# Kernel tuning notes

Hardware: AMD Instinct MI355X
Metric: run time of the kernel (lower is better)

Reference implementation:

```python
import jax, jax.numpy as jnp
import numpy as np

Y_SCALE = 1.0   # from init_kwargs
EPS = 1e-12     # matches torch F.normalize eps


def _l2_normalize(x):
    n = jnp.linalg.norm(x, axis=-1, keepdims=True)
    return x / jnp.maximum(n, EPS)


def _sequence_similarity(a, b):
    # a: [B, N, D], b: [B, M, D]
    a = _l2_normalize(a)
    b = _l2_normalize(b)
    cos_sims = jnp.einsum('bnd,bmd->bnm', a, b)  # [B, N, M]
    if cos_sims.shape[-1] > cos_sims.shape[-2]:
        max_sims = cos_sims.max(axis=-1)  # [B, N]
    else:
        max_sims = cos_sims.max(axis=-2)  # [B, M]
    return max_sims.mean(axis=-1)  # [B]


def setup_inputs() -> dict:
    key = jax.random.key(0)
    k1, k2, k3 = jax.random.split(key, 3)
    B, N, M, D = 16, 4096, 2048, 256
    x1 = jax.random.normal(k1, (B, N, D), dtype=jnp.float32)
    x2 = jax.random.normal(k2, (B, M, D), dtype=jnp.float32)
    y = jax.random.uniform(k3, (B,), dtype=jnp.float32)
    return {"x1": x1, "x2": x2, "y": y}


def reference(x1, x2, y):
    raw_sim_scores = _sequence_similarity(x1, x2)  # [B]
    losses = (raw_sim_scores - y) ** 2
    scales = jnp.where(y != 0.0, jnp.float32(Y_SCALE), jnp.float32(1.0))
    return (losses * scales).sum()
```

## Files before the change

### kernel.cpp

```cpp
#include <hip/hip_runtime.h>
#include <hip/hip_bf16.h>
#include <cstdint>
#include <cstddef>

#define BATCH 16
#define NROWS 4096
#define MROWS 2048
#define DDIM  256
#define NSPLIT 2
#define NCHUNKS 8

typedef __attribute__((ext_vector_type(8)))  int   i32x8;
typedef __attribute__((ext_vector_type(16))) float f32x16;

__global__ void __launch_bounds__(256) norm_cast(
    const float* __restrict__ x1, const float* __restrict__ x2,
    unsigned char* __restrict__ aout, unsigned char* __restrict__ bout) {
  const int wid  = threadIdx.x >> 6;
  const int lane = threadIdx.x & 63;
  const long long row = (long long)blockIdx.x * 4 + wid;
  const long long R1 = (long long)BATCH * NROWS;
  const long long R2 = (long long)BATCH * MROWS;
  if (row >= R1 + R2) return;
  const float* src; unsigned char* dst;
  if (row < R1) { src = x1 + row * DDIM; dst = aout + row * DDIM; }
  else { long long r2 = row - R1; src = x2 + r2 * DDIM; dst = bout + r2 * DDIM; }
  float4 v = ((const float4*)src)[lane];
  float ss = v.x*v.x + v.y*v.y + v.z*v.z + v.w*v.w;
  #pragma unroll
  for (int o = 32; o >= 1; o >>= 1) ss += __shfl_xor(ss, o, 64);
  float sc = 1.0f / fmaxf(sqrtf(ss), 1e-12f);
  int r = __builtin_amdgcn_cvt_pk_fp8_f32(v.x * sc, v.y * sc, 0, false);
  r = __builtin_amdgcn_cvt_pk_fp8_f32(v.z * sc, v.w * sc, r, true);
  ((unsigned int*)dst)[lane] = (unsigned int)r;
}

typedef __attribute__((address_space(1))) const void gas_t;
typedef __attribute__((address_space(3))) void las_t;
#define GLL16(g, l) __builtin_amdgcn_global_lds((gas_t*)(g), (las_t*)(l), 16, 0, 0)
#undef GLL16
#define GLL16(g, l) __builtin_amdgcn_global_load_lds((gas_t*)(g), (las_t*)(l), 16, 0, 0)

#define LDSA(S) (lds + ((S) << 14))
#define LDSB(S) (lds + 65536 + ((S) << 14))

static __device__ __forceinline__ i32x8 frag8(const char* slot, int row, int lane) {
  const int rb = (lane >> 1) & 3;
  const int ks = lane >> 5;
  const char* base = slot + row * 64;
  uint4 u0 = *(const uint4*)(base + ((((ks << 1) | 0) ^ rb) << 4));
  uint4 u1 = *(const uint4*)(base + ((((ks << 1) | 1) ^ rb) << 4));
  i32x8 r;
  r[0] = u0.x; r[1] = u0.y; r[2] = u0.z; r[3] = u0.w;
  r[4] = u1.x; r[5] = u1.y; r[6] = u1.z; r[7] = u1.w;
  return r;
}

__global__ void __launch_bounds__(512, 1) maxsim_fp8(
    const unsigned char* __restrict__ A,
    const unsigned char* __restrict__ Bm,
    float* __restrict__ partials)
{
  __shared__ __align__(16) char lds[131072];

  const int t = threadIdx.x;
  const int lane = t & 63;
  const int w = t >> 6;
  const int wr = w >> 2;
  const int wc = w & 3;
  const int l31 = lane & 31;

  const int hw = blockIdx.x;
  const int logical = (hw & 7) * 32 + (hw >> 3);
  const int mt = logical & 7;
  const int grp = logical >> 3;
  const int sp = grp & 1;
  const int bb = grp >> 1;

  const int m0 = mt * 256;
  const int nbase = sp * (NROWS / NSPLIT);

  const unsigned char* Aba = A  + (size_t)bb * NROWS * DDIM;
  const unsigned char* Bba = Bm + ((size_t)bb * MROWS + m0) * DDIM;

  const int r0 = (w * 2 + 0) * 16 + (lane >> 2);
  const int r1 = (w * 2 + 1) * 16 + (lane >> 2);
  const int sph = (((lane & 3) ^ ((lane >> 3) & 3)) << 4);
  const unsigned char* sA0 = Aba + (size_t)r0 * DDIM + sph;
  const unsigned char* sA1 = Aba + (size_t)r1 * DDIM + sph;
  const unsigned char* sB0 = Bba + (size_t)r0 * DDIM + sph;
  const unsigned char* sB1 = Bba + (size_t)r1 * DDIM + sph;
  const int l0 = (w * 2 + 0) * 1024 + lane * 16;
  const int l1 = (w * 2 + 1) * 1024 + lane * 16;

  #define STAGE_A(SLOT, OFF) do { \
    GLL16(sA0 + (OFF), (SLOT) + l0); GLL16(sA1 + (OFF), (SLOT) + l1); } while (0)
  #define STAGE_B(SLOT, OFF) do { \
    GLL16(sB0 + (OFF), (SLOT) + l0); GLL16(sB1 + (OFF), (SLOT) + l1); } while (0)

  f32x16 acc[4][2] = {};
  const f32x16 z16 = {};
  i32x8 af[4], bf[2];
  float cm[2] = {-INFINITY, -INFINITY};

  STAGE_A(LDSA(0), (size_t)nbase * DDIM + 0);
  STAGE_B(LDSB(0), 0);
  STAGE_B(LDSB(1), 64);
  STAGE_B(LDSB(2), 128);
  STAGE_B(LDSB(3), 192);
  STAGE_A(LDSA(1), (size_t)nbase * DDIM + 64);
  asm volatile("s_waitcnt vmcnt(8)" ::: "memory");
  asm volatile("s_barrier" ::: "memory");

  for (int nc = 0; nc < NCHUNKS; ++nc) {
    #pragma unroll
    for (int kt = 0; kt < 4; ++kt) {
      const char* sa = LDSA(kt);
      const char* sb = LDSB(kt);
      const int s2 = (kt + 2) & 3;
      const int nc2 = (kt < 2) ? nc : ((nc + 1) & (NCHUNKS - 1));
      const size_t offA2 = ((size_t)nbase + nc2 * 256) * DDIM + s2 * 64;

      #pragma unroll
      for (int nj = 0; nj < 2; ++nj)
        bf[nj] = frag8(sb, wc * 64 + nj * 32 + l31, lane);
      #pragma unroll
      for (int mi = 0; mi < 4; ++mi)
        af[mi] = frag8(sa, wr * 128 + mi * 32 + l31, lane);
      STAGE_A(LDSA(s2), offA2);
      #pragma unroll
      for (int mi = 0; mi < 4; ++mi)
        #pragma unroll
        for (int nj = 0; nj < 2; ++nj)
          acc[mi][nj] = __builtin_amdgcn_mfma_scale_f32_32x32x64_f8f6f4(
              af[mi], bf[nj], acc[mi][nj], 0, 0,
              0, 0x7F7F7F7F, 0, 0x7F7F7F7F);
      asm volatile("s_waitcnt vmcnt(2)" ::: "memory");
      asm volatile("s_barrier" ::: "memory");
    }
    #pragma unroll
    for (int nj = 0; nj < 2; ++nj) {
      float v = cm[nj];
      #pragma unroll
      for (int mi = 0; mi < 4; ++mi) {
        #pragma unroll
        for (int r = 0; r < 16; ++r) v = fmaxf(v, acc[mi][nj][r]);
        acc[mi][nj] = z16;
      }
      cm[nj] = v;
    }
  }

  asm volatile("s_waitcnt vmcnt(0)" ::: "memory");
  asm volatile("s_barrier" ::: "memory");
  #pragma unroll
  for (int nj = 0; nj < 2; ++nj)
    cm[nj] = fmaxf(cm[nj], __shfl_xor(cm[nj], 32, 64));
  float* cmax = (float*)lds;
  if (lane < 32) {
    cmax[wr * 256 + wc * 64 + l31]      = cm[0];
    cmax[wr * 256 + wc * 64 + 32 + l31] = cm[1];
  }
  __syncthreads();
  if (t < 256) {
    float v = fmaxf(cmax[t], cmax[256 + t]);
    partials[((size_t)sp * BATCH + bb) * MROWS + m0 + t] = v;
  }
}

__global__ void __launch_bounds__(256) batch_loss(
    const float* __restrict__ partials, const float* __restrict__ y,
    float* __restrict__ bloss) {
  __shared__ float red[4];
  const int b = blockIdx.x;
  const int t = threadIdx.x;
  const int lane = t & 63;
  const int w = t >> 6;
  float s = 0.0f;
  for (int m = t; m < MROWS; m += 256) {
    float v = partials[(size_t)b * MROWS + m];
    #pragma unroll
    for (int sp = 1; sp < NSPLIT; ++sp)
      v = fmaxf(v, partials[((size_t)sp * BATCH + b) * MROWS + m]);
    s += v;
  }
  #pragma unroll
  for (int o = 32; o >= 1; o >>= 1) s += __shfl_xor(s, o, 64);
  if (lane == 0) red[w] = s;
  __syncthreads();
  if (t == 0) {
    float sum = red[0] + red[1] + red[2] + red[3];
    float mean = sum / (float)MROWS;
    float yb = y[b];
    float d = mean - yb;
    bloss[b] = d * d;
  }
}

__global__ void __launch_bounds__(64) final_sum(
    const float* __restrict__ bloss, float* __restrict__ out) {
  const int t = threadIdx.x;
  float v = (t < BATCH) ? bloss[t] : 0.0f;
  #pragma unroll
  for (int o = 32; o >= 1; o >>= 1) v += __shfl_xor(v, o, 64);
  if (t == 0) out[0] = v;
}

extern "C" void kernel_launch(void* const* d_in, const int* in_sizes, int n_in,
                              void* d_out, int out_size, void* d_ws, size_t ws_size,
                              hipStream_t stream) {
  const float* x1 = (const float*)d_in[0];
  const float* x2 = (const float*)d_in[1];
  const float* y  = (const float*)d_in[2];
  float* out = (float*)d_out;

  unsigned char* aF8 = (unsigned char*)d_ws;
  unsigned char* bF8 = aF8 + (size_t)BATCH * NROWS * DDIM;
  float* partials = (float*)(bF8 + (size_t)BATCH * MROWS * DDIM);
  float* bloss = partials + (size_t)NSPLIT * BATCH * MROWS;

  const int totRows = BATCH * (NROWS + MROWS);
  norm_cast<<<(totRows + 3) / 4, 256, 0, stream>>>(x1, x2, aF8, bF8);
  maxsim_fp8<<<BATCH * 8 * NSPLIT, 512, 0, stream>>>(aF8, bF8, partials);
  batch_loss<<<BATCH, 256, 0, stream>>>(partials, y, bloss);
  final_sum<<<1, 64, 0, stream>>>(bloss, out);
}
```

Baseline: 54.16 us.

## Double-buffer LDS fragments in registers and deepen A prefetch to three stages

Deepens the global-to-LDS prefetch of A from two to three k-slices ahead. Adds ping-pong register fragment buffers so the LDS reads for the next k-tile are issued before the MFMAs of the current one, hiding LDS read latency behind matrix math. This costs more VGPRs and tightens the slot-reuse timing. A slot being overwritten while still being read would be a correctness hazard, since only one barrier per k-tile protects it.

```diff
diff --git a/kernel.cpp b/kernel.cpp
--- a/kernel.cpp
+++ b/kernel.cpp
@@ -37,8 +37,6 @@
 
 typedef __attribute__((address_space(1))) const void gas_t;
 typedef __attribute__((address_space(3))) void las_t;
-#define GLL16(g, l) __builtin_amdgcn_global_lds((gas_t*)(g), (las_t*)(l), 16, 0, 0)
-#undef GLL16
 #define GLL16(g, l) __builtin_amdgcn_global_load_lds((gas_t*)(g), (las_t*)(l), 16, 0, 0)
 
 #define LDSA(S) (lds + ((S) << 14))
@@ -100,7 +98,7 @@
 
   f32x16 acc[4][2] = {};
   const f32x16 z16 = {};
-  i32x8 af[4], bf[2];
+  i32x8 afP[4], bfP[2], afQ[4], bfQ[2];
   float cm[2] = {-INFINITY, -INFINITY};
 
   STAGE_A(LDSA(0), (size_t)nbase * DDIM + 0);
@@ -109,35 +107,45 @@
   STAGE_B(LDSB(2), 128);
   STAGE_B(LDSB(3), 192);
   STAGE_A(LDSA(1), (size_t)nbase * DDIM + 64);
-  asm volatile("s_waitcnt vmcnt(8)" ::: "memory");
+  STAGE_A(LDSA(2), (size_t)nbase * DDIM + 128);
+  asm volatile("s_waitcnt vmcnt(2)" ::: "memory");
   asm volatile("s_barrier" ::: "memory");
 
+  #pragma unroll
+  for (int nj = 0; nj < 2; ++nj)
+    bfP[nj] = frag8(LDSB(0), wc * 64 + nj * 32 + l31, lane);
+  #pragma unroll
+  for (int mi = 0; mi < 4; ++mi)
+    afP[mi] = frag8(LDSA(0), wr * 128 + mi * 32 + l31, lane);
+
+  #define KTILE(KT, CAF, CBF, NAF, NBF) do {                                       \
+    const int s3 = ((KT) + 3) & 3;                                                 \
+    const int nc3 = ((KT) == 0) ? nc : ((nc + 1) & (NCHUNKS - 1));                 \
+    const size_t offA3 = ((size_t)nbase + nc3 * 256) * DDIM + s3 * 64;             \
+    STAGE_A(LDSA(s3), offA3);                                                      \
+    const int s1 = ((KT) + 1) & 3;                                                 \
+    _Pragma("unroll")                                                              \
+    for (int nj = 0; nj < 2; ++nj)                                                 \
+      NBF[nj] = frag8(LDSB(s1), wc * 64 + nj * 32 + l31, lane);                    \
+    _Pragma("unroll")                                                              \
+    for (int mi = 0; mi < 4; ++mi)                                                 \
+      NAF[mi] = frag8(LDSA(s1), wr * 128 + mi * 32 + l31, lane);                   \
+    _Pragma("unroll")                                                              \
+    for (int mi = 0; mi < 4; ++mi)                                                 \
+      _Pragma("unroll")                                                            \
+      for (int nj = 0; nj < 2; ++nj)                                               \
+        acc[mi][nj] = __builtin_amdgcn_mfma_scale_f32_32x32x64_f8f6f4(             \
+            CAF[mi], CBF[nj], acc[mi][nj], 0, 0,                                   \
+            0, 0x7F7F7F7F, 0, 0x7F7F7F7F);              \
+    asm volatile("s_waitcnt vmcnt(2)" ::: "memory");                               \
+    asm volatile("s_barrier" ::: "memory");                                        \
+  } while (0)
+
   for (int nc = 0; nc < NCHUNKS; ++nc) {
-    #pragma unroll
-    for (int kt = 0; kt < 4; ++kt) {
-      const char* sa = LDSA(kt);
-      const char* sb = LDSB(kt);
-      const int s2 = (kt + 2) & 3;
-      const int nc2 = (kt < 2) ? nc : ((nc + 1) & (NCHUNKS - 1));
-      const size_t offA2 = ((size_t)nbase + nc2 * 256) * DDIM + s2 * 64;
-
-      #pragma unroll
-      for (int nj = 0; nj < 2; ++nj)
-        bf[nj] = frag8(sb, wc * 64 + nj * 32 + l31, lane);
-      #pragma unroll
-      for (int mi = 0; mi < 4; ++mi)
-        af[mi] = frag8(sa, wr * 128 + mi * 32 + l31, lane);
-      STAGE_A(LDSA(s2), offA2);
-      #pragma unroll
-      for (int mi = 0; mi < 4; ++mi)
-        #pragma unroll
-        for (int nj = 0; nj < 2; ++nj)
-          acc[mi][nj] = __builtin_amdgcn_mfma_scale_f32_32x32x64_f8f6f4(
-              af[mi], bf[nj], acc[mi][nj], 0, 0,
-              0, 0x7F7F7F7F, 0, 0x7F7F7F7F);
-      asm volatile("s_waitcnt vmcnt(2)" ::: "memory");
-      asm volatile("s_barrier" ::: "memory");
-    }
+    KTILE(0, afP, bfP, afQ, bfQ);
+    KTILE(1, afQ, bfQ, afP, bfP);
+    KTILE(2, afP, bfP, afQ, bfQ);
+    KTILE(3, afQ, bfQ, afP, bfP);
     #pragma unroll
     for (int nj = 0; nj < 2; ++nj) {
       float v = cm[nj];
@@ -150,6 +158,7 @@
       cm[nj] = v;
     }
   }
+  #undef KTILE
 
   asm volatile("s_waitcnt vmcnt(0)" ::: "memory");
   asm volatile("s_barrier" ::: "memory");
```

New measurement: 55.59 us. +2.7%, slower.
